# Kernel optimization log

Measured on AMD Instinct MI355X. Metric: run time of the kernel, lower is better.

Reference implementation:

```python
import jax, jax.numpy as jnp
import numpy as np

LEVELS = 3  # num_basis = 1 + 1 + 2 + 4 = 8


def _haar_basis(x):
    """Closed-form vectorized Haar basis, x: [B, F] raw inputs.

    Replaces the original nested per-feature/per-level/per-bucket mask loops:
    at each level only one bucket k = floor(u*freq) is active, with value
    +2^(level/2) on the left half of the bucket and -2^(level/2) on the right
    half (x == 1.0 falls in the right half of the last bucket, matching the
    torch edge-case handling).
    """
    u = (jnp.tanh(x) + 1.0) / 2.0  # normalize to [0, 1]
    cols = [jnp.ones_like(u)[..., None]]  # scaling function phi
    for level in range(LEVELS):
        freq = 2 ** level
        k = jnp.clip(jnp.floor(u * freq), 0, freq - 1).astype(jnp.int32)  # bucket idx
        mid = (k.astype(u.dtype) + 0.5) / freq
        amp = jnp.asarray(2.0 ** (level / 2), u.dtype)
        sign = jnp.where(u < mid, amp, -amp)  # [B, F]
        cols.append(jax.nn.one_hot(k, freq, dtype=u.dtype) * sign[..., None])
    return jnp.concatenate(cols, axis=-1)  # [B, F, num_basis]


def setup_inputs() -> dict:
    key = jax.random.key(0)
    k1, k2, k3 = jax.random.split(key, 3)
    B, F, O, NB = 32768, 1024, 64, 8
    x = jax.random.normal(k1, (B, F), dtype=jnp.float32)
    coeffs = jax.random.normal(k2, (F, O, NB), dtype=jnp.float32) * 0.05
    base_weight = jax.random.normal(k3, (F, O), dtype=jnp.float32) * 0.05
    return {"x": x, "coeffs": coeffs, "base_weight": base_weight}


def reference(x, coeffs, base_weight):
    basis = _haar_basis(x)                         # [B, F, NB]
    wave_out = jnp.einsum('bin,ion->bo', basis, coeffs)  # [B, O]
    out = wave_out + x @ base_weight               # residual path
    kl = jnp.zeros((1,), dtype=x.dtype)            # non-variational: kl = 0
    return (out, kl)
```

## Files before the change

### kernel.cpp

```cpp
#include <hip/hip_runtime.h>
#include <math.h>


typedef __attribute__((ext_vector_type(8))) short short8;
typedef __attribute__((ext_vector_type(4))) float f32x4;
typedef __attribute__((ext_vector_type(16))) float f32x16;

__device__ __forceinline__ unsigned int f2bf(float f) {
  unsigned int u = __float_as_uint(f);
  u += 0x7FFFu + ((u >> 16) & 1u);
  return u >> 16;
}

__device__ __forceinline__ void gen_basis(int j, unsigned int* d) {
  d[0] = (j < 4) ? 0x3F803F80u : 0xBF803F80u;
  unsigned int sq1 = (j & 2) ? 0xBFB5u : 0x3FB5u;
  d[1] = (j & 4) ? (sq1 << 16) : sq1;
  unsigned long long sd2 = (j & 1) ? 0xC000ull : 0x4000ull;
  unsigned long long d23 = sd2 << ((j & 6) << 3);
  d[2] = (unsigned int)d23;
  d[3] = (unsigned int)(d23 >> 32);
}

#define BARRIER() __asm__ volatile("s_waitcnt lgkmcnt(0)\n\ts_barrier" ::: "memory")
#define KEEP4(v) __asm__ volatile("" : "+v"((v).x), "+v"((v).y), "+v"((v).z), "+v"((v).w))

__device__ __forceinline__ void build_half(const float4& xq,
                                           uint4* __restrict__ dst, int h) {
  float xv[4] = {xq.x, xq.y, xq.z, xq.w};
  float t8v[4];
  unsigned int bad = 0;
#pragma unroll
  for (int ff = 0; ff < 4; ++ff) {
    float e = __expf(2.0f * xv[ff]);
    float r = __builtin_amdgcn_rcpf(e + 1.0f);
    float t8 = __builtin_fmaf(-8.0f, r, 8.0f);
    float rn = rintf(t8);
    if (fabsf(t8 - rn) < 3e-5f) bad |= 1u << ff;
    t8v[ff] = t8;
  }
  if (__builtin_expect(bad != 0, 0)) {
#pragma unroll
    for (int ff = 0; ff < 4; ++ff)
      if (bad & (1u << ff)) {
        float tf = (float)tanh((double)xv[ff]);
        t8v[ff] = ((tf + 1.0f) * 0.5f) * 8.0f;
      }
  }
  unsigned int dw[18];
#pragma unroll
  for (int p = 0; p < 2; ++p) {
    int je = (int)t8v[2 * p];     je = je > 7 ? 7 : je;
    int jo = (int)t8v[2 * p + 1]; jo = jo > 7 ? 7 : jo;
    gen_basis(je, &dw[9 * p]);
    dw[9 * p + 4] = f2bf(xv[2 * p]) | (f2bf(xv[2 * p + 1]) << 16);
    gen_basis(jo, &dw[9 * p + 5]);
  }
  const int db = h ? 2 : 0;
  const int gb = h ? 5 : 0;
#pragma unroll
  for (int k = 0; k < 4; ++k) {
    uint4 qv;
    qv.x = dw[db + 4 * k];     qv.y = dw[db + 4 * k + 1];
    qv.z = dw[db + 4 * k + 2]; qv.w = dw[db + 4 * k + 3];
    dst[(gb + k) * 256] = qv;
  }
  uint2 hv;
  if (h) { hv.x = dw[0];  hv.y = dw[1];  }
  else   { hv.x = dw[16]; hv.y = dw[17]; }
  ((uint2*)(dst + 4 * 256))[h] = hv;
}

__global__ __launch_bounds__(256) void build_w(const float* __restrict__ coeffs,
                                               const float* __restrict__ bw,
                                               uint4* __restrict__ Wsw) {
  const int l = threadIdx.x & 63;
  const int t = threadIdx.x >> 6;
  const int g = blockIdx.x;
  const int c = g / 9, j = g - c * 9;
  const int u = t >> 1, nq = t & 1;
  const int R = c * 4 + 2 * u + (l >> 5);
  const int o = nq * 32 + (l & 31);
  unsigned int dwv[4];
#pragma unroll
  for (int jj = 0; jj < 8; ++jj) {
    int d = 8 * j + jj;
    int p = d / 18;
    int e = d - p * 18;
    int f, n;
    if (e < 8)       { f = 8 * R + 2 * p;     n = e; }
    else if (e == 8) { f = 8 * R + 2 * p;     n = 8; }
    else if (e == 9) { f = 8 * R + 2 * p + 1; n = 8; }
    else             { f = 8 * R + 2 * p + 1; n = e - 10; }
    float v = (n < 8) ? coeffs[(f * 64 + o) * 8 + n] : bw[f * 64 + o];
    unsigned int hh = f2bf(v);
    if (jj & 1) dwv[jj >> 1] |= hh << 16; else dwv[jj >> 1] = hh;
  }
  uint4 qq; qq.x = dwv[0]; qq.y = dwv[1]; qq.z = dwv[2]; qq.w = dwv[3];
  Wsw[(g * 4 + t) * 64 + l] = qq;
}

#define MFMA32(A, B, C) __builtin_amdgcn_mfma_f32_32x32x16_bf16( \
    __builtin_bit_cast(short8, (A)), __builtin_bit_cast(short8, (B)), (C), 0, 0, 0)

template <int NS>
__device__ __forceinline__ void run_main(const float* __restrict__ xrow,
                                         const uint4* __restrict__ Bsw,
                                         uint4* __restrict__ Albuf,
                                         f32x16& acc0, f32x16& acc1,
                                         int s0, int nq, int l, int wr_off, int h) {
  const int hi = l >> 5;
  const int l31 = l & 31;
  float4 xa = *(const float4*)(xrow);
  build_half(xa, Albuf + wr_off, h);
  xa = *(const float4*)(xrow + 32);
  BARRIER();

  for (int c = 0; c < 32; ++c) {
    uint4* cur = Albuf + (c & 1) * 2304;
    uint4* nxt = Albuf + ((c + 1) & 1) * 2304;
    uint4 Bv[NS][2];
#pragma unroll
    for (int i = 0; i < NS; ++i) {
      const uint4* wp = Bsw + (size_t)(((c * 9 + s0 + 4 * i) * 4 + nq) * 64) + l;
      Bv[i][0] = wp[0];
      Bv[i][1] = wp[128];
    }
    if (c + 1 < 32) {
      build_half(xa, nxt + wr_off, h);
      if (c + 2 < 32) xa = *(const float4*)(xrow + (c + 2) * 32);
    }
#pragma unroll
    for (int i = 0; i < NS; ++i) { KEEP4(Bv[i][0]); KEEP4(Bv[i][1]); }
#pragma unroll
    for (int i = 0; i < NS; ++i) {
      const int s = s0 + 4 * i;
      const uint4* rb = cur + s * 256 + hi * 64 + l31;
      uint4 a00 = rb[0];
      uint4 a01 = rb[32];
      uint4 a10 = rb[128];
      uint4 a11 = rb[160];
      acc0 = MFMA32(a00, Bv[i][0], acc0);
      acc0 = MFMA32(a10, Bv[i][1], acc0);
      acc1 = MFMA32(a01, Bv[i][0], acc1);
      acc1 = MFMA32(a11, Bv[i][1], acc1);
    }
    BARRIER();
  }
}

__global__ __launch_bounds__(512, 4) void wavelet_gemm(const float* __restrict__ x,
                                                       const uint4* __restrict__ Bsw,
                                                       float* __restrict__ out,
                                                       int out_size) {
  __shared__ uint4 Albuf[2 * 9 * 256];
  const int tid = threadIdx.x;
  const int l = tid & 63;
  const int w = tid >> 6;
  const int nq = w & 1;
  const int ks = w >> 1;
  const int r = w & 3;
  const int h = w >> 2;
  const int m = l;
  const long rowbase = (long)blockIdx.x * 64;
  const int wr_off = r * 64 + m;

  f32x16 acc0 = {};
  f32x16 acc1 = {};

  const float* xrow = x + (rowbase + m) * 1024 + r * 8 + h * 4;

  if (ks == 0) run_main<3>(xrow, Bsw, Albuf, acc0, acc1, 0, nq, l, wr_off, h);
  else         run_main<2>(xrow, Bsw, Albuf, acc0, acc1, ks, nq, l, wr_off, h);

  float* P = (float*)Albuf;
  float* Pk = P + ks * 4096;
  const int col   = nq * 32 + (l & 31);
  const int rbase = 4 * (l >> 5);
#pragma unroll
  for (int rg = 0; rg < 16; ++rg) {
    const int grow = (rg & 3) + 8 * (rg >> 2) + rbase;
    Pk[grow * 64 + col]        = acc0[rg];
    Pk[(grow + 32) * 64 + col] = acc1[rg];
  }
  BARRIER();

  float* og = out + (size_t)rowbase * 64;
  const int row = tid >> 3;
  const int cb  = (tid & 7) * 8;
  f32x4 v0 = *(const f32x4*)(P + row * 64 + cb);
  f32x4 v1 = *(const f32x4*)(P + row * 64 + cb + 4);
#pragma unroll
  for (int k = 1; k < 4; ++k) {
    v0 = v0 + *(const f32x4*)(P + k * 4096 + row * 64 + cb);
    v1 = v1 + *(const f32x4*)(P + k * 4096 + row * 64 + cb + 4);
  }
  *(f32x4*)(og + row * 64 + cb)     = v0;
  *(f32x4*)(og + row * 64 + cb + 4) = v1;
  if (blockIdx.x == 0 && tid == 0) out[out_size - 1] = 0.0f;
}

extern "C" void kernel_launch(void* const* d_in, const int* in_sizes, int n_in,
                              void* d_out, int out_size, void* d_ws, size_t ws_size,
                              hipStream_t stream) {
  const float* x      = (const float*)d_in[0];
  const float* coeffs = (const float*)d_in[1];
  const float* bw     = (const float*)d_in[2];
  uint4* Wsw = (uint4*)d_ws;
  float* out = (float*)d_out;

  build_w<<<288, 256, 0, stream>>>(coeffs, bw, Wsw);
  wavelet_gemm<<<512, 512, 0, stream>>>(x, (const uint4*)Wsw, out, out_size);
}
```

Before: 225.3 us.

## Warp-specialize GEMM into producer waves building basis and consumer MFMA waves

Splits the 8 waves of each block into 4 producer waves that compute the Haar basis and bf16 x tiles into LDS, and 4 consumer waves that only issue MFMAs. The consumers run at raised priority via s_setprio. The K split across consumers drops from 4 to 2, so the final reduction sums only two partials. The LDS and weight layouts change to one basis run per feature, which simplifies the weight-packing index math. This aims to overlap the transcendental-heavy basis build with the matrix math. The cost is that half the waves do no MFMA work and each consumer wave now holds more B fragments in registers.

```diff
diff --git a/kernel.cpp b/kernel.cpp
--- a/kernel.cpp
+++ b/kernel.cpp
@@ -23,15 +23,14 @@
 }
 
 #define BARRIER() __asm__ volatile("s_waitcnt lgkmcnt(0)\n\ts_barrier" ::: "memory")
-#define KEEP4(v) __asm__ volatile("" : "+v"((v).x), "+v"((v).y), "+v"((v).z), "+v"((v).w))
-
-__device__ __forceinline__ void build_half(const float4& xq,
-                                           uint4* __restrict__ dst, int h) {
-  float xv[4] = {xq.x, xq.y, xq.z, xq.w};
-  float t8v[4];
+
+__device__ __forceinline__ void build_run(const float4& xa, const float4& xb,
+                                          uint4* __restrict__ dst) {
+  float xv[8] = {xa.x, xa.y, xa.z, xa.w, xb.x, xb.y, xb.z, xb.w};
+  float t8v[8];
   unsigned int bad = 0;
 #pragma unroll
-  for (int ff = 0; ff < 4; ++ff) {
+  for (int ff = 0; ff < 8; ++ff) {
     float e = __expf(2.0f * xv[ff]);
     float r = __builtin_amdgcn_rcpf(e + 1.0f);
     float t8 = __builtin_fmaf(-8.0f, r, 8.0f);
@@ -41,34 +40,26 @@
   }
   if (__builtin_expect(bad != 0, 0)) {
 #pragma unroll
-    for (int ff = 0; ff < 4; ++ff)
+    for (int ff = 0; ff < 8; ++ff)
       if (bad & (1u << ff)) {
         float tf = (float)tanh((double)xv[ff]);
         t8v[ff] = ((tf + 1.0f) * 0.5f) * 8.0f;
       }
   }
-  unsigned int dw[18];
-#pragma unroll
-  for (int p = 0; p < 2; ++p) {
-    int je = (int)t8v[2 * p];     je = je > 7 ? 7 : je;
-    int jo = (int)t8v[2 * p + 1]; jo = jo > 7 ? 7 : jo;
-    gen_basis(je, &dw[9 * p]);
-    dw[9 * p + 4] = f2bf(xv[2 * p]) | (f2bf(xv[2 * p + 1]) << 16);
-    gen_basis(jo, &dw[9 * p + 5]);
-  }
-  const int db = h ? 2 : 0;
-  const int gb = h ? 5 : 0;
-#pragma unroll
-  for (int k = 0; k < 4; ++k) {
-    uint4 qv;
-    qv.x = dw[db + 4 * k];     qv.y = dw[db + 4 * k + 1];
-    qv.z = dw[db + 4 * k + 2]; qv.w = dw[db + 4 * k + 3];
-    dst[(gb + k) * 256] = qv;
-  }
-  uint2 hv;
-  if (h) { hv.x = dw[0];  hv.y = dw[1];  }
-  else   { hv.x = dw[16]; hv.y = dw[17]; }
-  ((uint2*)(dst + 4 * 256))[h] = hv;
+#pragma unroll
+  for (int ff = 0; ff < 8; ++ff) {
+    int j = (int)t8v[ff]; j = j > 7 ? 7 : j;
+    unsigned int d[4];
+    gen_basis(j, d);
+    uint4 qv; qv.x = d[0]; qv.y = d[1]; qv.z = d[2]; qv.w = d[3];
+    dst[ff * 256] = qv;
+  }
+  uint4 xq;
+  xq.x = f2bf(xv[0]) | (f2bf(xv[1]) << 16);
+  xq.y = f2bf(xv[2]) | (f2bf(xv[3]) << 16);
+  xq.z = f2bf(xv[4]) | (f2bf(xv[5]) << 16);
+  xq.w = f2bf(xv[6]) | (f2bf(xv[7]) << 16);
+  dst[8 * 256] = xq;
 }
 
 __global__ __launch_bounds__(256) void build_w(const float* __restrict__ coeffs,
@@ -84,14 +75,9 @@
   unsigned int dwv[4];
 #pragma unroll
   for (int jj = 0; jj < 8; ++jj) {
-    int d = 8 * j + jj;
-    int p = d / 18;
-    int e = d - p * 18;
     int f, n;
-    if (e < 8)       { f = 8 * R + 2 * p;     n = e; }
-    else if (e == 8) { f = 8 * R + 2 * p;     n = 8; }
-    else if (e == 9) { f = 8 * R + 2 * p + 1; n = 8; }
-    else             { f = 8 * R + 2 * p + 1; n = e - 10; }
+    if (j < 8) { f = 8 * R + j;  n = jj; }
+    else       { f = 8 * R + jj; n = 8;  }
     float v = (n < 8) ? coeffs[(f * 64 + o) * 8 + n] : bw[f * 64 + o];
     unsigned int hh = f2bf(v);
     if (jj & 1) dwv[jj >> 1] |= hh << 16; else dwv[jj >> 1] = hh;
@@ -104,37 +90,26 @@
     __builtin_bit_cast(short8, (A)), __builtin_bit_cast(short8, (B)), (C), 0, 0, 0)
 
 template <int NS>
-__device__ __forceinline__ void run_main(const float* __restrict__ xrow,
-                                         const uint4* __restrict__ Bsw,
-                                         uint4* __restrict__ Albuf,
-                                         f32x16& acc0, f32x16& acc1,
-                                         int s0, int nq, int l, int wr_off, int h) {
+__device__ __forceinline__ void mfma_main(const uint4* __restrict__ Bsw,
+                                          const uint4* __restrict__ Albuf,
+                                          f32x16& acc0, f32x16& acc1,
+                                          int ks, int nq, int l) {
   const int hi = l >> 5;
   const int l31 = l & 31;
-  float4 xa = *(const float4*)(xrow);
-  build_half(xa, Albuf + wr_off, h);
-  xa = *(const float4*)(xrow + 32);
   BARRIER();
-
   for (int c = 0; c < 32; ++c) {
-    uint4* cur = Albuf + (c & 1) * 2304;
-    uint4* nxt = Albuf + ((c + 1) & 1) * 2304;
+    const uint4* cur = Albuf + (c & 1) * 2304;
     uint4 Bv[NS][2];
 #pragma unroll
     for (int i = 0; i < NS; ++i) {
-      const uint4* wp = Bsw + (size_t)(((c * 9 + s0 + 4 * i) * 4 + nq) * 64) + l;
+      const uint4* wp = Bsw + (size_t)(((c * 9 + ks + 2 * i) * 4 + nq) * 64) + l;
       Bv[i][0] = wp[0];
       Bv[i][1] = wp[128];
     }
-    if (c + 1 < 32) {
-      build_half(xa, nxt + wr_off, h);
-      if (c + 2 < 32) xa = *(const float4*)(xrow + (c + 2) * 32);
-    }
-#pragma unroll
-    for (int i = 0; i < NS; ++i) { KEEP4(Bv[i][0]); KEEP4(Bv[i][1]); }
+    __builtin_amdgcn_s_setprio(1);
 #pragma unroll
     for (int i = 0; i < NS; ++i) {
-      const int s = s0 + 4 * i;
+      const int s = ks + 2 * i;
       const uint4* rb = cur + s * 256 + hi * 64 + l31;
       uint4 a00 = rb[0];
       uint4 a01 = rb[32];
@@ -145,6 +120,7 @@
       acc1 = MFMA32(a01, Bv[i][0], acc1);
       acc1 = MFMA32(a11, Bv[i][1], acc1);
     }
+    __builtin_amdgcn_s_setprio(0);
     BARRIER();
   }
 }
@@ -157,44 +133,56 @@
   const int tid = threadIdx.x;
   const int l = tid & 63;
   const int w = tid >> 6;
-  const int nq = w & 1;
-  const int ks = w >> 1;
-  const int r = w & 3;
-  const int h = w >> 2;
-  const int m = l;
   const long rowbase = (long)blockIdx.x * 64;
-  const int wr_off = r * 64 + m;
-
-  f32x16 acc0 = {};
-  f32x16 acc1 = {};
-
-  const float* xrow = x + (rowbase + m) * 1024 + r * 8 + h * 4;
-
-  if (ks == 0) run_main<3>(xrow, Bsw, Albuf, acc0, acc1, 0, nq, l, wr_off, h);
-  else         run_main<2>(xrow, Bsw, Albuf, acc0, acc1, ks, nq, l, wr_off, h);
-
   float* P = (float*)Albuf;
-  float* Pk = P + ks * 4096;
-  const int col   = nq * 32 + (l & 31);
-  const int rbase = 4 * (l >> 5);
-#pragma unroll
-  for (int rg = 0; rg < 16; ++rg) {
-    const int grow = (rg & 3) + 8 * (rg >> 2) + rbase;
-    Pk[grow * 64 + col]        = acc0[rg];
-    Pk[(grow + 32) * 64 + col] = acc1[rg];
-  }
-  BARRIER();
+
+  if (w < 4) {
+    const int nq = w & 1;
+    const int ks = w >> 1;
+    f32x16 acc0 = {};
+    f32x16 acc1 = {};
+    if (ks == 0) mfma_main<5>(Bsw, Albuf, acc0, acc1, 0, nq, l);
+    else         mfma_main<4>(Bsw, Albuf, acc0, acc1, 1, nq, l);
+    float* Pk = P + ks * 4096;
+    const int col   = nq * 32 + (l & 31);
+    const int rbase = 4 * (l >> 5);
+#pragma unroll
+    for (int rg = 0; rg < 16; ++rg) {
+      const int grow = (rg & 3) + 8 * (rg >> 2) + rbase;
+      Pk[grow * 64 + col]        = acc0[rg];
+      Pk[(grow + 32) * 64 + col] = acc1[rg];
+    }
+    BARRIER();
+  } else {
+    const int r = w - 4;
+    uint4* wr0 = Albuf + r * 64 + l;
+    const float* xrow = x + (rowbase + l) * 1024 + r * 8;
+    float4 xa = *(const float4*)(xrow);
+    float4 xb = *(const float4*)(xrow + 4);
+    build_run(xa, xb, wr0);
+    xa = *(const float4*)(xrow + 32);
+    xb = *(const float4*)(xrow + 36);
+    BARRIER();
+    for (int c = 0; c < 32; ++c) {
+      if (c + 1 < 32) {
+        build_run(xa, xb, Albuf + ((c + 1) & 1) * 2304 + r * 64 + l);
+        if (c + 2 < 32) {
+          xa = *(const float4*)(xrow + (c + 2) * 32);
+          xb = *(const float4*)(xrow + (c + 2) * 32 + 4);
+        }
+      }
+      BARRIER();
+    }
+    BARRIER();
+  }
 
   float* og = out + (size_t)rowbase * 64;
   const int row = tid >> 3;
   const int cb  = (tid & 7) * 8;
   f32x4 v0 = *(const f32x4*)(P + row * 64 + cb);
   f32x4 v1 = *(const f32x4*)(P + row * 64 + cb + 4);
-#pragma unroll
-  for (int k = 1; k < 4; ++k) {
-    v0 = v0 + *(const f32x4*)(P + k * 4096 + row * 64 + cb);
-    v1 = v1 + *(const f32x4*)(P + k * 4096 + row * 64 + cb + 4);
-  }
+  v0 = v0 + *(const f32x4*)(P + 4096 + row * 64 + cb);
+  v1 = v1 + *(const f32x4*)(P + 4096 + row * 64 + cb + 4);
   *(f32x4*)(og + row * 64 + cb)     = v0;
   *(f32x4*)(og + row * 64 + cb + 4) = v1;
   if (blockIdx.x == 0 && tid == 0) out[out_size - 1] = 0.0f;
```

After: 225.3 us. About the same (-0.0%).
